# Kernel optimization log

Hardware: AMD Instinct MI355X
Metric: run time of the kernel (lower is better)

## Reference

```python
import jax, jax.numpy as jnp
import numpy as np

D_MODEL = 1024
N_HEADS = 16
MAX_SEQ = 1024
BATCH = 4

def _first_primes(n):
    limit = n * 15
    sieve = np.ones(limit, dtype=bool)
    sieve[:2] = False
    for i in range(2, int(limit ** 0.5) + 1):
        if sieve[i]:
            sieve[i * i::i] = False
    return np.flatnonzero(sieve)[:n]

def _pi_attention_bias(n_heads, max_seq_len):
    # bias[h, t, s] = 0.1 * sin(prime[h]*pi * (t - s) / max_seq_len)
    primes = _first_primes(n_heads).astype(np.float32)
    freqs = primes * np.pi  # [H]
    pos = np.arange(max_seq_len, dtype=np.float32)
    pos_diff = pos[:, None] - pos[None, :]  # [T, T]
    bias = np.sin(freqs[:, None, None] * pos_diff[None] / max_seq_len) * 0.1
    return jnp.asarray(bias, dtype=jnp.float32)

def setup_inputs() -> dict:
    key = jax.random.key(0)
    ks = jax.random.split(key, 8)
    D = D_MODEL
    xavier = (6.0 / (D + D)) ** 0.5
    inp = {
        'x': jax.random.normal(ks[0], (BATCH, MAX_SEQ, D), dtype=jnp.float32),
        'Wq': jax.random.uniform(ks[1], (D, D), jnp.float32, -xavier, xavier),
        'bq': jnp.zeros((D,), jnp.float32),
        'Wk': jax.random.uniform(ks[2], (D, D), jnp.float32, -xavier, xavier),
        'bk': jnp.zeros((D,), jnp.float32),
        'Wv': jax.random.uniform(ks[3], (D, D), jnp.float32, -xavier, xavier),
        'bv': jnp.zeros((D,), jnp.float32),
        'Wo': jax.random.uniform(ks[4], (D, D), jnp.float32, -xavier, xavier),
        'bo': jnp.zeros((D,), jnp.float32),
        'pi_bias': _pi_attention_bias(N_HEADS, MAX_SEQ),
        'bias_scale': jnp.asarray(0.1, jnp.float32),
        'spectral_alpha': jnp.asarray(1.0, jnp.float32),
    }
    return inp

def reference(x, Wq, bq, Wk, bk, Wv, bv, Wo, bo, pi_bias, bias_scale, spectral_alpha):
    B, T, D = x.shape
    H = N_HEADS
    hd = D // H
    scale = 1.0 / (hd ** 0.5)

    def split_heads(y):
        return y.reshape(B, T, H, hd).transpose(0, 2, 1, 3)  # [B,H,T,hd]

    q = split_heads(x @ Wq + bq)
    k = split_heads(x @ Wk + bk)
    v = split_heads(x @ Wv + bv)

    # spectral filter along the time axis (use_spectral and T > 4)
    freqs = jnp.fft.fftfreq(T).astype(jnp.float32)  # [T]
    filt = jnp.exp(-jnp.abs(spectral_alpha) * jnp.abs(freqs))[None, None, :, None]
    q = jnp.fft.ifft(jnp.fft.fft(q, axis=2, norm='ortho') * filt, axis=2, norm='ortho').real
    k = jnp.fft.ifft(jnp.fft.fft(k, axis=2, norm='ortho') * filt, axis=2, norm='ortho').real

    scores = jnp.einsum('bhtd,bhsd->bhts', q, k) * scale
    scores = scores + bias_scale * pi_bias[None, :, :T, :T]
    attn = jax.nn.softmax(scores, axis=-1)  # dropout is identity in eval
    out = jnp.einsum('bhts,bhsd->bhtd', attn, v)
    out = out.transpose(0, 2, 1, 3).reshape(B, T, D)
    return out @ Wo + bo
```

## Files before the change

kernel.cpp:

```cpp
#include <hip/hip_runtime.h>
#include <hip/hip_bf16.h>

typedef __bf16 bf16x8 __attribute__((ext_vector_type(8)));
typedef float f32x4 __attribute__((ext_vector_type(4)));

#define OFF_GMAT   0x10000ULL
#define OFF_XB     0x210000ULL
#define OFF_XBT    0xA10000ULL
#define OFF_XF     0x1210000ULL
#define OFF_WQT    0x1A10000ULL
#define OFF_WKT    0x1C10000ULL
#define OFF_WVT    0x1E10000ULL
#define OFF_WOT    0x2010000ULL
#define OFF_KB     0x2210000ULL
#define OFF_VTB    0x2A10000ULL

static __device__ __forceinline__ unsigned short f2bf(float f) {
  union { float f; unsigned int u; } v; v.f = f;
  unsigned int r = v.u + 0x7FFFu + ((v.u >> 16) & 1u);
  return (unsigned short)(r >> 16);
}

static __device__ __forceinline__ void g2l16(const unsigned short* g, unsigned short* l) {
  __builtin_amdgcn_global_load_lds(
      (const __attribute__((address_space(1))) unsigned int*)g,
      (__attribute__((address_space(3))) unsigned int*)l, 16, 0, 0);
}

__constant__ float PRIMES_F[16] = {2.f, 3.f, 5.f, 7.f, 11.f, 13.f, 17.f, 19.f,
                                   23.f, 29.f, 31.f, 37.f, 41.f, 43.f, 47.f, 53.f};

__global__ __launch_bounds__(256) void k_prep(
    const float* __restrict__ x, const float* __restrict__ w0,
    const float* __restrict__ w1, const float* __restrict__ w2,
    const float* __restrict__ w3, const float* __restrict__ alpha_p,
    unsigned short* __restrict__ xb, unsigned short* __restrict__ xbT,
    unsigned short* __restrict__ Wout, unsigned short* __restrict__ Gm) {
  __shared__ float tile[32][33];
  const int z = blockIdx.z;
  const int r0 = blockIdx.y * 32, c0 = blockIdx.x * 32;
  if (z == 8) {
    const int tx = threadIdx.x & 31, ty = threadIdx.x >> 5;
    const float alpha = fmaxf(fabsf(alpha_p[0]), 1e-6f);
    const float q = __expf(-alpha * (1.f / 1024.f));
    const float q512 = __expf(-alpha * 0.5f);
    #pragma unroll
    for (int i = 0; i < 4; i++) {
      const int t = r0 + ty + 8 * i, s = c0 + tx;
      const int d = (t - s) & 1023;
      float s_, c_;
      __sincosf((float)d * (6.28318530717958647692f / 1024.f), &s_, &c_);
      const float sgn = (d & 1) ? -1.f : 1.f;
      const float Nr = q * c_ - q512 * sgn, Ni = q * s_;
      const float Wr = 1.f - q * c_, Wi = -q * s_;
      const float sum = (Nr * Wr + Ni * Wi) / (Wr * Wr + Wi * Wi);
      const float gd = (1.f + q512 * sgn + 2.f * sum) * (1.f / 1024.f);
      Gm[(long)t * 1024 + s] = f2bf(gd);
    }
    return;
  }
  const bool isX = z < 4;
  const float* in = isX ? (x + ((long)z << 20))
                        : (z == 4 ? w0 : z == 5 ? w1 : z == 6 ? w2 : w3);
  const long ooff = isX ? ((long)z << 20) : ((long)(z - 4) << 20);
  const int ty = threadIdx.x >> 3;
  const int c4 = (threadIdx.x & 7) * 4;
  float4 v = *(const float4*)(in + (long)(r0 + ty) * 1024 + c0 + c4);
  if (isX) {
    ushort4 o; o.x = f2bf(v.x); o.y = f2bf(v.y); o.z = f2bf(v.z); o.w = f2bf(v.w);
    *(ushort4*)(xb + ooff + (long)(r0 + ty) * 1024 + c0 + c4) = o;
  }
  tile[ty][c4 + 0] = v.x; tile[ty][c4 + 1] = v.y;
  tile[ty][c4 + 2] = v.z; tile[ty][c4 + 3] = v.w;
  __syncthreads();
  unsigned short* outT = isX ? xbT : Wout;
  ushort4 o;
  o.x = f2bf(tile[c4 + 0][ty]); o.y = f2bf(tile[c4 + 1][ty]);
  o.z = f2bf(tile[c4 + 2][ty]); o.w = f2bf(tile[c4 + 3][ty]);
  *(ushort4*)(outT + ooff + (long)(c0 + ty) * 1024 + r0 + c4) = o;
}

#define GEMM_CORE(A_, Bt_, ACC_)                                                     \
  const int tid = threadIdx.x, l = tid & 63, wid = tid >> 6;                         \
  const int lr = l & 15, lg = l >> 4;                                                \
  const int wm = (wid >> 1) * 64, wn = (wid & 1) * 64;                               \
  const int scol = ((l & 7) ^ (l >> 3)) * 8;                                         \
  const unsigned short* Ag = A_ + (long)(m0 + wid * 32 + (l >> 3)) * 1024 + scol;    \
  const unsigned short* Bg = Bt_ + (long)(n0 + wid * 32 + (l >> 3)) * 1024 + scol;   \
  const int xk = (lr & 7) << 4;                                                      \
  const int co[2] = {(0 + lg * 16) ^ xk, (64 + lg * 16) ^ xk};                       \
  {                                                                                  \
    _Pragma("unroll")                                                                \
    for (int c = 0; c < 4; c++) {                                                    \
      g2l16(Ag + (long)c * 8192, &As[0][wid * 2048 + c * 512]);                      \
      g2l16(Bg + (long)c * 8192, &Bs[0][wid * 2048 + c * 512]);                      \
    }                                                                                \
    Ag += 64; Bg += 64;                                                              \
  }                                                                                  \
  __syncthreads();                                                                   \
  for (int t = 0; t < 16; ++t) {                                                     \
    const int cur = t & 1;                                                           \
    if (t < 15) {                                                                    \
      const int nxt = cur ^ 1;                                                       \
      _Pragma("unroll")                                                              \
      for (int c = 0; c < 4; c++) {                                                  \
        g2l16(Ag + (long)c * 8192, &As[nxt][wid * 2048 + c * 512]);                  \
        g2l16(Bg + (long)c * 8192, &Bs[nxt][wid * 2048 + c * 512]);                  \
      }                                                                              \
      Ag += 64; Bg += 64;                                                            \
      asm volatile("s_waitcnt vmcnt(8)" ::: "memory");                               \
    } else {                                                                         \
      asm volatile("s_waitcnt vmcnt(0)" ::: "memory");                               \
    }                                                                                \
    __builtin_amdgcn_s_barrier();                                                    \
    __builtin_amdgcn_sched_barrier(0);                                               \
    const char* Ab = (const char*)&As[cur][0];                                       \
    const char* Bb = (const char*)&Bs[cur][0];                                       \
    _Pragma("unroll")                                                                \
    for (int ks = 0; ks < 2; ks++) {                                                 \
      bf16x8 af[4], bfr[4];                                                          \
      _Pragma("unroll")                                                              \
      for (int mf = 0; mf < 4; mf++)                                                 \
        af[mf] = *(const bf16x8*)(Ab + (wm + mf * 16 + lr) * 128 + co[ks]);          \
      _Pragma("unroll")                                                              \
      for (int nf = 0; nf < 4; nf++)                                                 \
        bfr[nf] = *(const bf16x8*)(Bb + (wn + nf * 16 + lr) * 128 + co[ks]);         \
      _Pragma("unroll")                                                              \
      for (int mf = 0; mf < 4; mf++)                                                 \
        _Pragma("unroll")                                                            \
        for (int nf = 0; nf < 4; nf++)                                               \
          ACC_[mf][nf] = __builtin_amdgcn_mfma_f32_16x16x32_bf16(af[mf], bfr[nf],    \
                                                                 ACC_[mf][nf], 0, 0, 0); \
    }                                                                                \
    __builtin_amdgcn_sched_barrier(0);                                               \
    __builtin_amdgcn_s_barrier();                                                    \
  }

__global__ __launch_bounds__(256) void k_gemm5(
    const unsigned short* __restrict__ A, const unsigned short* __restrict__ Bt,
    const float* __restrict__ bias, const float* __restrict__ bias2,
    unsigned short* __restrict__ Cv, unsigned short* __restrict__ Cv2) {
  __shared__ __align__(16) unsigned short As[2][128 * 64];
  __shared__ __align__(16) unsigned short Bs[2][128 * 64];
  const int orig = (blockIdx.x & 7) * 64 + (blockIdx.x >> 3);
  const int m0 = (orig & 31) * 128, n0 = (orig >> 5) * 128;
  f32x4 acc[4][4] = {};
  GEMM_CORE(A, Bt, acc)
  #pragma unroll
  for (int nf = 0; nf < 4; nf++) {
    const int n = n0 + wn + nf * 16 + lr;
    const float bb = (n < 1024) ? bias[n] : bias2[n - 1024];
    unsigned short* Cd = (n < 1024) ? Cv : Cv2;
    #pragma unroll
    for (int mf = 0; mf < 4; mf++) {
      const int mb = m0 + wm + mf * 16 + lg * 4;
      #pragma unroll
      for (int r = 0; r < 4; r++)
        Cd[(long)(mb + r) * 1024 + (n & 1023)] = f2bf(acc[mf][nf][r] + bb);
    }
  }
}

__global__ __launch_bounds__(256) void k_fv(
    const unsigned short* __restrict__ Gm, const unsigned short* __restrict__ xbT,
    const unsigned short* __restrict__ WvT, const unsigned short* __restrict__ xb,
    const float* __restrict__ bv, unsigned short* __restrict__ Xf,
    unsigned short* __restrict__ Vtb) {
  __shared__ __align__(16) unsigned short As[2][128 * 64];
  __shared__ __align__(16) unsigned short Bs[2][128 * 64];
  const bool isV = blockIdx.x < 256;
  const int inner = blockIdx.x & 255;
  const int o = (inner & 7) * 32 + (inner >> 3);
  const int m0 = (o & 7) * 128, n0 = (o >> 3) * 128;
  const unsigned short* A_ = isV ? WvT : Gm;
  const unsigned short* Bt_ = isV ? xb : xbT;
  const int nk = isV ? 16 : 4;
  const int ktbase = isV ? 0 : ((m0 - 64) & 1023);
  const int tid = threadIdx.x, l = tid & 63, wid = tid >> 6;
  const int lr = l & 15, lg = l >> 4;
  const int wm = (wid >> 1) * 64, wn = (wid & 1) * 64;
  const int scol = ((l & 7) ^ (l >> 3)) * 8;
  const unsigned short* Ag = A_ + (long)(m0 + wid * 32 + (l >> 3)) * 1024 + scol;
  const unsigned short* Bg = Bt_ + (long)(n0 + wid * 32 + (l >> 3)) * 1024 + scol;
  const int xk = (lr & 7) << 4;
  const int co[2] = {(0 + lg * 16) ^ xk, (64 + lg * 16) ^ xk};
  {
    #pragma unroll
    for (int c = 0; c < 4; c++) {
      g2l16(Ag + (long)c * 8192 + ktbase, &As[0][wid * 2048 + c * 512]);
      g2l16(Bg + (long)c * 8192 + ktbase, &Bs[0][wid * 2048 + c * 512]);
    }
  }
  __syncthreads();
  f32x4 acc[4][4] = {};
  for (int t = 0; t < nk; ++t) {
    const int cur = t & 1;
    if (t < nk - 1) {
      const int nxt = cur ^ 1;
      const int kt = (ktbase + ((t + 1) << 6)) & 1023;
      #pragma unroll
      for (int c = 0; c < 4; c++) {
        g2l16(Ag + (long)c * 8192 + kt, &As[nxt][wid * 2048 + c * 512]);
        g2l16(Bg + (long)c * 8192 + kt, &Bs[nxt][wid * 2048 + c * 512]);
      }
      asm volatile("s_waitcnt vmcnt(8)" ::: "memory");
    } else {
      asm volatile("s_waitcnt vmcnt(0)" ::: "memory");
    }
    __builtin_amdgcn_s_barrier();
    __builtin_amdgcn_sched_barrier(0);
    const char* Ab = (const char*)&As[cur][0];
    const char* Bb = (const char*)&Bs[cur][0];
    #pragma unroll
    for (int ks = 0; ks < 2; ks++) {
      bf16x8 af[4], bfr[4];
      #pragma unroll
      for (int mf = 0; mf < 4; mf++)
        af[mf] = *(const bf16x8*)(Ab + (wm + mf * 16 + lr) * 128 + co[ks]);
      #pragma unroll
      for (int nf = 0; nf < 4; nf++)
        bfr[nf] = *(const bf16x8*)(Bb + (wn + nf * 16 + lr) * 128 + co[ks]);
      #pragma unroll
      for (int mf = 0; mf < 4; mf++)
        #pragma unroll
        for (int nf = 0; nf < 4; nf++)
          acc[mf][nf] = __builtin_amdgcn_mfma_f32_16x16x32_bf16(af[mf], bfr[nf], acc[mf][nf], 0, 0, 0);
    }
    __builtin_amdgcn_sched_barrier(0);
    __builtin_amdgcn_s_barrier();
  }
  #pragma unroll
  for (int nf = 0; nf < 4; nf++) {
    const int n = n0 + wn + nf * 16 + lr;
    #pragma unroll
    for (int mf = 0; mf < 4; mf++) {
      const int mb = wm + mf * 16 + lg * 4;
      #pragma unroll
      for (int r = 0; r < 4; r++) {
        const int m = m0 + mb + r;
        float v = acc[mf][nf][r];
        if (isV) {
          Vtb[(long)m * 4096 + n] = f2bf(v + bv[m]);
        } else {
          Xf[(long)((n & ~1023) + m) * 1024 + (n & 1023)] = f2bf(v);
        }
      }
    }
  }
}

__global__ __launch_bounds__(256) void k_gemmO(
    const unsigned short* __restrict__ A, const unsigned short* __restrict__ Bt,
    const float* __restrict__ bias, float* __restrict__ C) {
  __shared__ __align__(16) unsigned short As[2][64 * 64];
  __shared__ __align__(16) unsigned short Bs[2][128 * 64];
  const int orig = (blockIdx.x & 7) * 64 + (blockIdx.x >> 3);
  const int m0 = (orig & 63) * 64, n0 = (orig >> 6) * 128;
  const int tid = threadIdx.x, l = tid & 63, wid = tid >> 6;
  const int lr = l & 15, lg = l >> 4;
  const int wm = (wid >> 1) * 32, wn = (wid & 1) * 64;
  const int scol = ((l & 7) ^ (l >> 3)) * 8;
  const unsigned short* Ag = A + (long)(m0 + wid * 16 + (l >> 3)) * 1024 + scol;
  const unsigned short* Bg = Bt + (long)(n0 + wid * 32 + (l >> 3)) * 1024 + scol;
  const int xk = (lr & 7) << 4;
  const int co[2] = {(0 + lg * 16) ^ xk, (64 + lg * 16) ^ xk};
  {
    #pragma unroll
    for (int c = 0; c < 2; c++) g2l16(Ag + (long)c * 8192, &As[0][wid * 1024 + c * 512]);
    #pragma unroll
    for (int c = 0; c < 4; c++) g2l16(Bg + (long)c * 8192, &Bs[0][wid * 2048 + c * 512]);
    Ag += 64; Bg += 64;
  }
  __syncthreads();
  f32x4 acc[2][4] = {};
  for (int t = 0; t < 16; ++t) {
    const int cur = t & 1;
    if (t < 15) {
      const int nxt = cur ^ 1;
      #pragma unroll
      for (int c = 0; c < 2; c++) g2l16(Ag + (long)c * 8192, &As[nxt][wid * 1024 + c * 512]);
      #pragma unroll
      for (int c = 0; c < 4; c++) g2l16(Bg + (long)c * 8192, &Bs[nxt][wid * 2048 + c * 512]);
      Ag += 64; Bg += 64;
      asm volatile("s_waitcnt vmcnt(6)" ::: "memory");
    } else {
      asm volatile("s_waitcnt vmcnt(0)" ::: "memory");
    }
    __builtin_amdgcn_s_barrier();
    __builtin_amdgcn_sched_barrier(0);
    const char* Ab = (const char*)&As[cur][0];
    const char* Bb = (const char*)&Bs[cur][0];
    #pragma unroll
    for (int ks = 0; ks < 2; ks++) {
      bf16x8 af[2], bfr[4];
      #pragma unroll
      for (int mf = 0; mf < 2; mf++)
        af[mf] = *(const bf16x8*)(Ab + (wm + mf * 16 + lr) * 128 + co[ks]);
      #pragma unroll
      for (int nf = 0; nf < 4; nf++)
        bfr[nf] = *(const bf16x8*)(Bb + (wn + nf * 16 + lr) * 128 + co[ks]);
      #pragma unroll
      for (int mf = 0; mf < 2; mf++)
        #pragma unroll
        for (int nf = 0; nf < 4; nf++)
          acc[mf][nf] = __builtin_amdgcn_mfma_f32_16x16x32_bf16(af[mf], bfr[nf], acc[mf][nf], 0, 0, 0);
    }
    __builtin_amdgcn_sched_barrier(0);
    __builtin_amdgcn_s_barrier();
  }
  #pragma unroll
  for (int nf = 0; nf < 4; nf++) {
    const int n = n0 + wn + nf * 16 + lr;
    const float bb = bias[n];
    #pragma unroll
    for (int mf = 0; mf < 2; mf++) {
      const int mb = m0 + wm + mf * 16 + lg * 4;
      #pragma unroll
      for (int r = 0; r < 4; r++)
        C[(long)(mb + r) * 1024 + n] = acc[mf][nf][r] + bb;
    }
  }
}

__global__ __launch_bounds__(512) void k_attn(
    const unsigned short* __restrict__ Qb, const unsigned short* __restrict__ Kb,
    const unsigned short* __restrict__ Vtb,
    const float* __restrict__ bias_scale_p, unsigned short* __restrict__ Ob) {
  __shared__ __align__(16) unsigned short Kbuf[3][4096];
  __shared__ __align__(16) unsigned short Vbuf[3][4096];
  __shared__ __align__(16) unsigned short Ps[8][16 * 64];
  const int bid = blockIdx.x;
  const int qt = (bid >> 3) & 7;
  const int hb = ((bid >> 6) << 3) | (bid & 7);
  const int h = hb & 15, b = hb >> 4;
  const int tid = threadIdx.x, l = tid & 63, wid = tid >> 6;
  const int lr = l & 15, lg = l >> 4;
  const int q0 = qt * 128;
  const float LOG2E = 1.44269504088896f;
  const float c10 = bias_scale_p[0] * 0.1f * LOG2E;
  const float k1 = 0.125f * LOG2E;
  const float fh = PRIMES_F[h] * 3.14159265358979323846f;
  const unsigned short* Vth = Vtb + (long)h * 64 * 4096 + b * 1024;
  const int xk = (lr & 7) << 4;
  const int co[2] = {(0 + lg * 16) ^ xk, (64 + lg * 16) ^ xk};
  const int scol = ((l & 7) ^ (l >> 3)) * 8;

  const unsigned short* kg = Kb + (long)(b * 1024 + wid * 8 + (l >> 3)) * 1024 + h * 64 + scol;
  const unsigned short* vg = Vth + (long)(wid * 8 + (l >> 3)) * 4096 + scol;
  unsigned short* kls = &Kbuf[0][0];
  unsigned short* vls = &Vbuf[0][0];
  #define STAGE_TO(BI) \
    { g2l16(kg, kls + (BI) * 4096 + wid * 512); \
      g2l16(vg, vls + (BI) * 4096 + wid * 512); \
      kg += 64 * 1024; vg += 64; }

  STAGE_TO(0);
  STAGE_TO(1);

  bf16x8 af[2];
  #pragma unroll
  for (int ks = 0; ks < 2; ks++)
    af[ks] = *(const bf16x8*)(
        &Qb[(long)(b * 1024 + q0 + wid * 16 + lr) * 1024 + h * 64 + ks * 32 + lg * 8]);

  float st2[4], ct2[4];
  #pragma unroll
  for (int r = 0; r < 4; r++) {
    float tt = (float)(q0 + wid * 16 + lg * 4 + r);
    float s_, c_;
    __sincosf(fh * tt * (1.f / 1024.f), &s_, &c_);
    st2[r] = c10 * s_;
    ct2[r] = c10 * c_;
  }
  float ss4[4], cs4[4], sd, cd;
  __sincosf(fh * (1.f / 16.f), &sd, &cd);
  #pragma unroll
  for (int nf = 0; nf < 4; nf++)
    __sincosf(fh * (float)(nf * 16 + lr) * (1.f / 1024.f), &ss4[nf], &cs4[nf]);

  f32x4 acc_o[4] = {};
  float pden[4] = {};
  int cur = 0, stg = 2;
  __syncthreads();

  for (int it = 0; it < 16; ++it) {
    if (it < 15) {
      asm volatile("s_waitcnt vmcnt(2)" ::: "memory");
    } else {
      asm volatile("s_waitcnt vmcnt(0)" ::: "memory");
    }
    __builtin_amdgcn_s_barrier();
    __builtin_amdgcn_sched_barrier(0);
    if (it < 14) { STAGE_TO(stg); }
    const char* Kbb = (const char*)kls + cur * 8192;
    const char* Vbb = (const char*)vls + cur * 8192;
    f32x4 accs[4] = {};
    #pragma unroll
    for (int ks = 0; ks < 2; ks++) {
      bf16x8 bfr[4];
      #pragma unroll
      for (int nf = 0; nf < 4; nf++)
        bfr[nf] = *(const bf16x8*)(Kbb + (nf * 16 + lr) * 128 + co[ks]);
      __builtin_amdgcn_s_setprio(1);
      #pragma unroll
      for (int nf = 0; nf < 4; nf++)
        accs[nf] = __builtin_amdgcn_mfma_f32_16x16x32_bf16(af[ks], bfr[nf], accs[nf], 0, 0, 0);
      __builtin_amdgcn_s_setprio(0);
    }
    char* Pw = (char*)&Ps[wid][0];
    #pragma unroll
    for (int nf = 0; nf < 4; nf++) {
      #pragma unroll
      for (int r = 0; r < 4; r++) {
        float v = fmaf(accs[nf][r], k1, fmaf(st2[r], cs4[nf], -ct2[r] * ss4[nf]));
        float p;
        asm("v_exp_f32 %0, %1" : "=v"(p) : "v"(v));
        pden[r] += p;
        union { float f; unsigned int u; } pu; pu.f = p;
        const int prow = lg * 4 + r;
        *(unsigned short*)(Pw + prow * 128 + ((nf * 32 + lr * 2) ^ ((prow & 7) << 4))) =
            (unsigned short)((pu.u + 0x8000u) >> 16);
      }
    }
    #pragma unroll
    for (int ks = 0; ks < 2; ks++) {
      bf16x8 pa = *(const bf16x8*)(Pw + lr * 128 + co[ks]);
      bf16x8 vb[4];
      #pragma unroll
      for (int nf = 0; nf < 4; nf++)
        vb[nf] = *(const bf16x8*)(Vbb + (nf * 16 + lr) * 128 + co[ks]);
      __builtin_amdgcn_s_setprio(1);
      #pragma unroll
      for (int nf = 0; nf < 4; nf++)
        acc_o[nf] = __builtin_amdgcn_mfma_f32_16x16x32_bf16(pa, vb[nf], acc_o[nf], 0, 0, 0);
      __builtin_amdgcn_s_setprio(0);
    }
    #pragma unroll
    for (int nf = 0; nf < 4; nf++) {
      float c_ = cs4[nf] * cd - ss4[nf] * sd;
      ss4[nf] = ss4[nf] * cd + cs4[nf] * sd;
      cs4[nf] = c_;
    }
    cur = (cur == 2) ? 0 : cur + 1;
    stg = (stg == 2) ? 0 : stg + 1;
  }
  #undef STAGE_TO
  #pragma unroll
  for (int r = 0; r < 4; r++) {
    float dsum = pden[r];
    #pragma unroll
    for (int off = 1; off < 16; off <<= 1) dsum += __shfl_xor(dsum, off, 64);
    pden[r] = 1.0f / dsum;
  }
  const int tg = q0 + wid * 16 + lg * 4;
  #pragma unroll
  for (int nf = 0; nf < 4; nf++) {
    const int dd = nf * 16 + lr;
    #pragma unroll
    for (int r = 0; r < 4; r++) {
      float val = acc_o[nf][r] * pden[r];
      Ob[(long)(b * 1024 + tg + r) * 1024 + h * 64 + dd] = f2bf(val);
    }
  }
}

extern "C" void kernel_launch(void* const* d_in, const int* in_sizes, int n_in,
                              void* d_out, int out_size, void* d_ws, size_t ws_size,
                              hipStream_t stream) {
  const float* x   = (const float*)d_in[0];
  const float* Wq  = (const float*)d_in[1];
  const float* bq  = (const float*)d_in[2];
  const float* Wk  = (const float*)d_in[3];
  const float* bk  = (const float*)d_in[4];
  const float* Wv  = (const float*)d_in[5];
  const float* bv  = (const float*)d_in[6];
  const float* Wo  = (const float*)d_in[7];
  const float* bo  = (const float*)d_in[8];
  const float* bsc = (const float*)d_in[10];
  const float* alp = (const float*)d_in[11];
  char* ws = (char*)d_ws;
  unsigned short* Gm  = (unsigned short*)(ws + OFF_GMAT);
  unsigned short* xb  = (unsigned short*)(ws + OFF_XB);
  unsigned short* xbT = (unsigned short*)(ws + OFF_XBT);
  unsigned short* Xf  = (unsigned short*)(ws + OFF_XF);
  unsigned short* WqT = (unsigned short*)(ws + OFF_WQT);
  unsigned short* WvT = (unsigned short*)(ws + OFF_WVT);
  unsigned short* WoT = (unsigned short*)(ws + OFF_WOT);
  unsigned short* Qb  = xbT;
  unsigned short* Kb  = (unsigned short*)(ws + OFF_KB);
  unsigned short* Vtb = (unsigned short*)(ws + OFF_VTB);
  unsigned short* Ob  = Xf;

  k_prep<<<dim3(32, 32, 9), 256, 0, stream>>>(x, Wq, Wk, Wv, Wo, alp, xb, xbT, WqT, Gm);
  k_fv<<<512, 256, 0, stream>>>(Gm, xbT, WvT, xb, bv, Xf, Vtb);
  k_gemm5<<<512, 256, 0, stream>>>(Xf, WqT, bq, bk, Qb, Kb);
  k_attn<<<512, 512, 0, stream>>>(Qb, Kb, Vtb, bsc, Ob);
  k_gemmO<<<512, 256, 0, stream>>>(Ob, WoT, bo, (float*)d_out);
}
```

Baseline: 117.7 us.

## Fuse four post-prep kernels into one cooperative persistent kernel with grid syncs

Replaces the separate V/filter GEMM, QK projection GEMM, attention and output GEMM launches with a single cooperative kernel of 256 blocks × 512 threads, separated by grid-wide syncs. Each block processes two work units per phase, and the GEMMs are rewritten with 8-wave 128x128 tiles and single-buffered LDS loads. This removes launch gaps and tail effects between kernels. The cost is grid.sync overhead, fewer blocks in flight, and the loss of the double-buffered pipelining in the GEMMs. The old multi-kernel path is kept as a fallback if the cooperative launch fails.

```diff
diff --git a/kernel.cpp b/kernel.cpp
--- a/kernel.cpp
+++ b/kernel.cpp
@@ -1,5 +1,7 @@
 #include <hip/hip_runtime.h>
 #include <hip/hip_bf16.h>
+#include <hip/hip_cooperative_groups.h>
+namespace cg = cooperative_groups;
 
 typedef __bf16 bf16x8 __attribute__((ext_vector_type(8)));
 typedef float f32x4 __attribute__((ext_vector_type(4)));
@@ -9,7 +11,6 @@
 #define OFF_XBT    0xA10000ULL
 #define OFF_XF     0x1210000ULL
 #define OFF_WQT    0x1A10000ULL
-#define OFF_WKT    0x1C10000ULL
 #define OFF_WVT    0x1E10000ULL
 #define OFF_WOT    0x2010000ULL
 #define OFF_KB     0x2210000ULL
@@ -78,6 +79,298 @@
   o.x = f2bf(tile[c4 + 0][ty]); o.y = f2bf(tile[c4 + 1][ty]);
   o.z = f2bf(tile[c4 + 2][ty]); o.w = f2bf(tile[c4 + 3][ty]);
   *(ushort4*)(outT + ooff + (long)(c0 + ty) * 1024 + r0 + c4) = o;
+}
+
+__device__ __forceinline__ void gemm8w128(
+    unsigned short* As, unsigned short* Bs,
+    const unsigned short* A_, const unsigned short* Bt_,
+    int m0, int n0, int nk, int ktbase, f32x4 (&acc)[4][2],
+    int l, int wid, int lr, int lg) {
+  const int wm = (wid >> 2) * 64, wn = (wid & 3) * 32;
+  const int scol = ((l & 7) ^ (l >> 3)) * 8;
+  const unsigned short* Ag = A_ + (long)(m0 + wid * 16 + (l >> 3)) * 1024 + scol;
+  const unsigned short* Bg = Bt_ + (long)(n0 + wid * 16 + (l >> 3)) * 1024 + scol;
+  const int xk = (lr & 7) << 4;
+  const int co[2] = {(lg * 16) ^ xk, (64 + lg * 16) ^ xk};
+  for (int t = 0; t < nk; ++t) {
+    const int kt = (ktbase + (t << 6)) & 1023;
+    __syncthreads();
+    g2l16(Ag + kt, As + wid * 1024);
+    g2l16(Ag + 8 * 1024 + kt, As + wid * 1024 + 512);
+    g2l16(Bg + kt, Bs + wid * 1024);
+    g2l16(Bg + 8 * 1024 + kt, Bs + wid * 1024 + 512);
+    __syncthreads();
+    const char* Ab = (const char*)As;
+    const char* Bb = (const char*)Bs;
+    #pragma unroll
+    for (int ks = 0; ks < 2; ks++) {
+      bf16x8 af[4], bfr[2];
+      #pragma unroll
+      for (int mf = 0; mf < 4; mf++)
+        af[mf] = *(const bf16x8*)(Ab + (wm + mf * 16 + lr) * 128 + co[ks]);
+      #pragma unroll
+      for (int nf = 0; nf < 2; nf++)
+        bfr[nf] = *(const bf16x8*)(Bb + (wn + nf * 16 + lr) * 128 + co[ks]);
+      #pragma unroll
+      for (int mf = 0; mf < 4; mf++)
+        #pragma unroll
+        for (int nf = 0; nf < 2; nf++)
+          acc[mf][nf] = __builtin_amdgcn_mfma_f32_16x16x32_bf16(af[mf], bfr[nf], acc[mf][nf], 0, 0, 0);
+    }
+  }
+}
+
+__global__ __launch_bounds__(512, 2) void k_mega(
+    const unsigned short* __restrict__ Gm, const unsigned short* __restrict__ xbT,
+    const unsigned short* __restrict__ WvT, const unsigned short* __restrict__ xb,
+    const float* __restrict__ bv, unsigned short* __restrict__ Xf,
+    unsigned short* __restrict__ Vtb, const unsigned short* __restrict__ WqkT,
+    const float* __restrict__ bq, const float* __restrict__ bk,
+    unsigned short* __restrict__ Qb, unsigned short* __restrict__ Kb,
+    const float* __restrict__ bias_scale_p, unsigned short* __restrict__ Ob,
+    const unsigned short* __restrict__ WoT, const float* __restrict__ bo,
+    float* __restrict__ Cout) {
+  __shared__ __align__(16) unsigned short smem[32768];
+  cg::grid_group grid = cg::this_grid();
+  const int bid = blockIdx.x;
+  const int tid = threadIdx.x, l = tid & 63, wid = tid >> 6;
+  const int lr = l & 15, lg = l >> 4;
+
+  for (int u = 0; u < 2; ++u) {
+    const bool isV = (u == 0);
+    const int o = (bid & 7) * 32 + (bid >> 3);
+    const int m0 = (o & 7) * 128, n0 = (o >> 3) * 128;
+    const int nk = isV ? 16 : 4;
+    const int ktbase = isV ? 0 : ((m0 - 64) & 1023);
+    f32x4 acc[4][2] = {};
+    gemm8w128(smem, smem + 8192, isV ? WvT : Gm, isV ? xb : xbT,
+              m0, n0, nk, ktbase, acc, l, wid, lr, lg);
+    const int wm = (wid >> 2) * 64, wn = (wid & 3) * 32;
+    #pragma unroll
+    for (int nf = 0; nf < 2; nf++) {
+      const int n = n0 + wn + nf * 16 + lr;
+      #pragma unroll
+      for (int mf = 0; mf < 4; mf++) {
+        const int mb = wm + mf * 16 + lg * 4;
+        #pragma unroll
+        for (int r = 0; r < 4; r++) {
+          const int m = m0 + mb + r;
+          float v = acc[mf][nf][r];
+          if (isV) Vtb[(long)m * 4096 + n] = f2bf(v + bv[m]);
+          else     Xf[(long)((n & ~1023) + m) * 1024 + (n & 1023)] = f2bf(v);
+        }
+      }
+    }
+  }
+  grid.sync();
+
+  for (int u = 0; u < 2; ++u) {
+    const int uid = bid + (u << 8);
+    const int o = (uid & 7) * 64 + (uid >> 3);
+    const int m0 = (o & 31) * 128, n0 = (o >> 5) * 128;
+    f32x4 acc[4][2] = {};
+    gemm8w128(smem, smem + 8192, Xf, WqkT, m0, n0, 16, 0, acc, l, wid, lr, lg);
+    const int wm = (wid >> 2) * 64, wn = (wid & 3) * 32;
+    #pragma unroll
+    for (int nf = 0; nf < 2; nf++) {
+      const int n = n0 + wn + nf * 16 + lr;
+      const float bb = (n < 1024) ? bq[n] : bk[n - 1024];
+      unsigned short* Cd = (n < 1024) ? Qb : Kb;
+      #pragma unroll
+      for (int mf = 0; mf < 4; mf++) {
+        const int mb = m0 + wm + mf * 16 + lg * 4;
+        #pragma unroll
+        for (int r = 0; r < 4; r++)
+          Cd[(long)(mb + r) * 1024 + (n & 1023)] = f2bf(acc[mf][nf][r] + bb);
+      }
+    }
+  }
+  grid.sync();
+
+  {
+    unsigned short* kls = smem;
+    unsigned short* vls = smem + 12288;
+    unsigned short* Psb = smem + 24576;
+    const float LOG2E = 1.44269504088896f;
+    const float c10 = bias_scale_p[0] * 0.1f * LOG2E;
+    const float k1 = 0.125f * LOG2E;
+    for (int u = 0; u < 2; ++u) {
+      const int uid = bid + (u << 8);
+      const int qt = (uid >> 3) & 7;
+      const int hb = ((uid >> 6) << 3) | (uid & 7);
+      const int h = hb & 15, b = hb >> 4;
+      const int q0 = qt * 128;
+      const float fh = PRIMES_F[h] * 3.14159265358979323846f;
+      const unsigned short* Vth = Vtb + (long)h * 64 * 4096 + b * 1024;
+      const int xk = (lr & 7) << 4;
+      const int co[2] = {(lg * 16) ^ xk, (64 + lg * 16) ^ xk};
+      const int scol = ((l & 7) ^ (l >> 3)) * 8;
+      const unsigned short* kg = Kb + (long)(b * 1024 + wid * 8 + (l >> 3)) * 1024 + h * 64 + scol;
+      const unsigned short* vg = Vth + (long)(wid * 8 + (l >> 3)) * 4096 + scol;
+      #define STAGE_TO(BI) \
+        { g2l16(kg, kls + (BI) * 4096 + wid * 512); \
+          g2l16(vg, vls + (BI) * 4096 + wid * 512); \
+          kg += 64 * 1024; vg += 64; }
+      __syncthreads();
+      STAGE_TO(0);
+      STAGE_TO(1);
+      bf16x8 af[2];
+      #pragma unroll
+      for (int ks = 0; ks < 2; ks++)
+        af[ks] = *(const bf16x8*)(
+            &Qb[(long)(b * 1024 + q0 + wid * 16 + lr) * 1024 + h * 64 + ks * 32 + lg * 8]);
+      float st2[4], ct2[4];
+      #pragma unroll
+      for (int r = 0; r < 4; r++) {
+        float tt = (float)(q0 + wid * 16 + lg * 4 + r);
+        float s_, c_;
+        __sincosf(fh * tt * (1.f / 1024.f), &s_, &c_);
+        st2[r] = c10 * s_;
+        ct2[r] = c10 * c_;
+      }
+      float ss4[4], cs4[4], sd, cd;
+      __sincosf(fh * (1.f / 16.f), &sd, &cd);
+      #pragma unroll
+      for (int nf = 0; nf < 4; nf++)
+        __sincosf(fh * (float)(nf * 16 + lr) * (1.f / 1024.f), &ss4[nf], &cs4[nf]);
+      f32x4 acc_o[4] = {};
+      float pden[4] = {};
+      int cur = 0, stg = 2;
+      __syncthreads();
+      for (int it = 0; it < 16; ++it) {
+        if (it < 15) {
+          asm volatile("s_waitcnt vmcnt(2)" ::: "memory");
+        } else {
+          asm volatile("s_waitcnt vmcnt(0)" ::: "memory");
+        }
+        __builtin_amdgcn_s_barrier();
+        __builtin_amdgcn_sched_barrier(0);
+        if (it < 14) { STAGE_TO(stg); }
+        const char* Kbb = (const char*)kls + cur * 8192;
+        const char* Vbb = (const char*)vls + cur * 8192;
+        f32x4 accs[4] = {};
+        #pragma unroll
+        for (int ks = 0; ks < 2; ks++) {
+          bf16x8 bfr[4];
+          #pragma unroll
+          for (int nf = 0; nf < 4; nf++)
+            bfr[nf] = *(const bf16x8*)(Kbb + (nf * 16 + lr) * 128 + co[ks]);
+          __builtin_amdgcn_s_setprio(1);
+          #pragma unroll
+          for (int nf = 0; nf < 4; nf++)
+            accs[nf] = __builtin_amdgcn_mfma_f32_16x16x32_bf16(af[ks], bfr[nf], accs[nf], 0, 0, 0);
+          __builtin_amdgcn_s_setprio(0);
+        }
+        char* Pw = (char*)(Psb + wid * 1024);
+        #pragma unroll
+        for (int nf = 0; nf < 4; nf++) {
+          #pragma unroll
+          for (int r = 0; r < 4; r++) {
+            float v = fmaf(accs[nf][r], k1, fmaf(st2[r], cs4[nf], -ct2[r] * ss4[nf]));
+            float p;
+            asm("v_exp_f32 %0, %1" : "=v"(p) : "v"(v));
+            pden[r] += p;
+            union { float f; unsigned int u; } pu; pu.f = p;
+            const int prow = lg * 4 + r;
+            *(unsigned short*)(Pw + prow * 128 + ((nf * 32 + lr * 2) ^ ((prow & 7) << 4))) =
+                (unsigned short)((pu.u + 0x8000u) >> 16);
+          }
+        }
+        #pragma unroll
+        for (int ks = 0; ks < 2; ks++) {
+          bf16x8 pa = *(const bf16x8*)(Pw + lr * 128 + co[ks]);
+          bf16x8 vb[4];
+          #pragma unroll
+          for (int nf = 0; nf < 4; nf++)
+            vb[nf] = *(const bf16x8*)(Vbb + (nf * 16 + lr) * 128 + co[ks]);
+          __builtin_amdgcn_s_setprio(1);
+          #pragma unroll
+          for (int nf = 0; nf < 4; nf++)
+            acc_o[nf] = __builtin_amdgcn_mfma_f32_16x16x32_bf16(pa, vb[nf], acc_o[nf], 0, 0, 0);
+          __builtin_amdgcn_s_setprio(0);
+        }
+        #pragma unroll
+        for (int nf = 0; nf < 4; nf++) {
+          float c_ = cs4[nf] * cd - ss4[nf] * sd;
+          ss4[nf] = ss4[nf] * cd + cs4[nf] * sd;
+          cs4[nf] = c_;
+        }
+        cur = (cur == 2) ? 0 : cur + 1;
+        stg = (stg == 2) ? 0 : stg + 1;
+      }
+      #undef STAGE_TO
+      #pragma unroll
+      for (int r = 0; r < 4; r++) {
+        float dsum = pden[r];
+        #pragma unroll
+        for (int off = 1; off < 16; off <<= 1) dsum += __shfl_xor(dsum, off, 64);
+        pden[r] = 1.0f / dsum;
+      }
+      const int tg = q0 + wid * 16 + lg * 4;
+      #pragma unroll
+      for (int nf = 0; nf < 4; nf++) {
+        const int dd = nf * 16 + lr;
+        #pragma unroll
+        for (int r = 0; r < 4; r++) {
+          float val = acc_o[nf][r] * pden[r];
+          Ob[(long)(b * 1024 + tg + r) * 1024 + h * 64 + dd] = f2bf(val);
+        }
+      }
+    }
+  }
+  grid.sync();
+
+  for (int u = 0; u < 2; ++u) {
+    const int uid = bid + (u << 8);
+    unsigned short* As = smem;
+    unsigned short* Bs = smem + 4096;
+    const int o = (uid & 7) * 64 + (uid >> 3);
+    const int m0 = (o & 63) * 64, n0 = (o >> 6) * 128;
+    const int wm = (wid >> 2) * 32, wn = (wid & 3) * 32;
+    const int scol = ((l & 7) ^ (l >> 3)) * 8;
+    const unsigned short* Ag = Ob + (long)(m0 + wid * 8 + (l >> 3)) * 1024 + scol;
+    const unsigned short* Bg = WoT + (long)(n0 + wid * 16 + (l >> 3)) * 1024 + scol;
+    const int xk = (lr & 7) << 4;
+    const int co[2] = {(lg * 16) ^ xk, (64 + lg * 16) ^ xk};
+    f32x4 acc[2][2] = {};
+    for (int t = 0; t < 16; ++t) {
+      const int kt = t << 6;
+      __syncthreads();
+      g2l16(Ag + kt, As + wid * 512);
+      g2l16(Bg + kt, Bs + wid * 1024);
+      g2l16(Bg + 8 * 1024 + kt, Bs + wid * 1024 + 512);
+      __syncthreads();
+      const char* Ab = (const char*)As;
+      const char* Bb = (const char*)Bs;
+      #pragma unroll
+      for (int ks = 0; ks < 2; ks++) {
+        bf16x8 af[2], bfr[2];
+        #pragma unroll
+        for (int mf = 0; mf < 2; mf++)
+          af[mf] = *(const bf16x8*)(Ab + (wm + mf * 16 + lr) * 128 + co[ks]);
+        #pragma unroll
+        for (int nf = 0; nf < 2; nf++)
+          bfr[nf] = *(const bf16x8*)(Bb + (wn + nf * 16 + lr) * 128 + co[ks]);
+        #pragma unroll
+        for (int mf = 0; mf < 2; mf++)
+          #pragma unroll
+          for (int nf = 0; nf < 2; nf++)
+            acc[mf][nf] = __builtin_amdgcn_mfma_f32_16x16x32_bf16(af[mf], bfr[nf], acc[mf][nf], 0, 0, 0);
+      }
+    }
+    #pragma unroll
+    for (int nf = 0; nf < 2; nf++) {
+      const int n = n0 + wn + nf * 16 + lr;
+      const float bb = bo[n];
+      #pragma unroll
+      for (int mf = 0; mf < 2; mf++) {
+        const int mb = m0 + wm + mf * 16 + lg * 4;
+        #pragma unroll
+        for (int r = 0; r < 4; r++)
+          Cout[(long)(mb + r) * 1024 + n] = acc[mf][nf][r] + bb;
+      }
+    }
+  }
 }
 
 #define GEMM_CORE(A_, Bt_, ACC_)                                                     \
@@ -239,11 +532,8 @@
       for (int r = 0; r < 4; r++) {
         const int m = m0 + mb + r;
         float v = acc[mf][nf][r];
-        if (isV) {
-          Vtb[(long)m * 4096 + n] = f2bf(v + bv[m]);
-        } else {
-          Xf[(long)((n & ~1023) + m) * 1024 + (n & 1023)] = f2bf(v);
-        }
+        if (isV) Vtb[(long)m * 4096 + n] = f2bf(v + bv[m]);
+        else     Xf[(long)((n & ~1023) + m) * 1024 + (n & 1023)] = f2bf(v);
       }
     }
   }
@@ -344,7 +634,6 @@
   const int xk = (lr & 7) << 4;
   const int co[2] = {(0 + lg * 16) ^ xk, (64 + lg * 16) ^ xk};
   const int scol = ((l & 7) ^ (l >> 3)) * 8;
-
   const unsigned short* kg = Kb + (long)(b * 1024 + wid * 8 + (l >> 3)) * 1024 + h * 64 + scol;
   const unsigned short* vg = Vth + (long)(wid * 8 + (l >> 3)) * 4096 + scol;
   unsigned short* kls = &Kbuf[0][0];
@@ -353,16 +642,13 @@
     { g2l16(kg, kls + (BI) * 4096 + wid * 512); \
       g2l16(vg, vls + (BI) * 4096 + wid * 512); \
       kg += 64 * 1024; vg += 64; }
-
   STAGE_TO(0);
   STAGE_TO(1);
-
   bf16x8 af[2];
   #pragma unroll
   for (int ks = 0; ks < 2; ks++)
     af[ks] = *(const bf16x8*)(
         &Qb[(long)(b * 1024 + q0 + wid * 16 + lr) * 1024 + h * 64 + ks * 32 + lg * 8]);
-
   float st2[4], ct2[4];
   #pragma unroll
   for (int r = 0; r < 4; r++) {
@@ -377,12 +663,10 @@
   #pragma unroll
   for (int nf = 0; nf < 4; nf++)
     __sincosf(fh * (float)(nf * 16 + lr) * (1.f / 1024.f), &ss4[nf], &cs4[nf]);
-
   f32x4 acc_o[4] = {};
   float pden[4] = {};
   int cur = 0, stg = 2;
   __syncthreads();
-
   for (int it = 0; it < 16; ++it) {
     if (it < 15) {
       asm volatile("s_waitcnt vmcnt(2)" ::: "memory");
@@ -490,10 +774,19 @@
   unsigned short* Kb  = (unsigned short*)(ws + OFF_KB);
   unsigned short* Vtb = (unsigned short*)(ws + OFF_VTB);
   unsigned short* Ob  = Xf;
+  float* outp = (float*)d_out;
 
   k_prep<<<dim3(32, 32, 9), 256, 0, stream>>>(x, Wq, Wk, Wv, Wo, alp, xb, xbT, WqT, Gm);
-  k_fv<<<512, 256, 0, stream>>>(Gm, xbT, WvT, xb, bv, Xf, Vtb);
-  k_gemm5<<<512, 256, 0, stream>>>(Xf, WqT, bq, bk, Qb, Kb);
-  k_attn<<<512, 512, 0, stream>>>(Qb, Kb, Vtb, bsc, Ob);
-  k_gemmO<<<512, 256, 0, stream>>>(Ob, WoT, bo, (float*)d_out);
-}
+
+  void* args[] = {&Gm, &xbT, &WvT, &xb, &bv, &Xf, &Vtb, &WqT, &bq, &bk,
+                  &Qb, &Kb, &bsc, &Ob, &WoT, &bo, &outp};
+  hipError_t ce = hipLaunchCooperativeKernel((void*)k_mega, dim3(256), dim3(512),
+                                             args, 0, stream);
+  if (ce != hipSuccess) {
+    (void)hipGetLastError();
+    k_fv   <<<512, 256, 0, stream>>>(Gm, xbT, WvT, xb, bv, Xf, Vtb);
+    k_gemm5<<<512, 256, 0, stream>>>(Xf, WqT, bq, bk, Qb, Kb);
+    k_attn <<<512, 512, 0, stream>>>(Qb, Kb, Vtb, bsc, Ob);
+    k_gemmO<<<512, 256, 0, stream>>>(Ob, WoT, bo, outp);
+  }
+}
```

Measured after the change: 248.0 us. 111% more time.
